# Performance work log

Measured on AMD Instinct MI355X. Metric: run time of the kernel, lower is better.

## Reference

```python
import jax, jax.numpy as jnp
import numpy as np

B, NPG, EPG = 128, 1000, 16000   # graphs, nodes per graph, edges per graph
D, K, C = 128, 64, 10            # assign_dim, clusters, classes


def gcn_conv(x, src, dst, W, b, N):
    """PyG GCNConv: add self-loops, symmetric D^-1/2 (A+I) D^-1/2 normalization."""
    loop = jnp.arange(N, dtype=src.dtype)
    s = jnp.concatenate([src, loop])
    d = jnp.concatenate([dst, loop])
    deg = jax.ops.segment_sum(jnp.ones_like(s, dtype=x.dtype), d, num_segments=N)
    dinv = jnp.where(deg > 0, jax.lax.rsqrt(deg), 0.0)
    xw = x @ W                                   # [N, out]
    msg = xw[s] * (dinv[s] * dinv[d])[:, None]   # gather + scale
    return jax.ops.segment_sum(msg, d, num_segments=N) + b


def setup_inputs() -> dict:
    N, E = B * NPG, B * EPG
    rng = np.random.default_rng(0)
    offs = np.repeat(np.arange(B, dtype=np.int32) * NPG, EPG)
    src = rng.integers(0, NPG, size=E).astype(np.int32) + offs
    dst = rng.integers(0, NPG, size=E).astype(np.int32) + offs
    edge_index = jnp.asarray(np.stack([src, dst]))          # [2, E], within-graph edges
    batch = jnp.repeat(jnp.arange(B, dtype=jnp.int32), NPG)  # [N], sorted graph ids

    ks = jax.random.split(jax.random.key(0), 8)
    sc = 0.05
    x = jax.random.normal(ks[0], (N, D), jnp.float32)
    return {
        "x": x,
        "edge_index": edge_index,
        "batch": batch,
        "W_pre": jax.random.normal(ks[1], (D, D), jnp.float32) * sc,
        "b_pre": jnp.zeros((D,), jnp.float32),
        "W_emb": jax.random.normal(ks[2], (D, D), jnp.float32) * sc,
        "b_emb": jnp.zeros((D,), jnp.float32),
        "W_asn": jax.random.normal(ks[3], (D, K), jnp.float32) * sc,
        "b_asn": jnp.zeros((K,), jnp.float32),
        "W1": jax.random.normal(ks[4], (D, D), jnp.float32) * sc,
        "b1": jnp.zeros((D,), jnp.float32),
        "W2": jax.random.normal(ks[5], (D, C), jnp.float32) * sc,
        "b2": jnp.zeros((C,), jnp.float32),
    }


def reference(x, edge_index, batch, W_pre, b_pre, W_emb, b_emb, W_asn, b_asn, W1, b1, W2, b2):
    N = x.shape[0]
    src, dst = edge_index[0], edge_index[1]

    # pre_conv + ReLU
    h = jax.nn.relu(gcn_conv(x, src, dst, W_pre, b_pre, N))

    # DiffPool: embed and assign GCNs
    NE = jax.nn.relu(gcn_conv(h, src, dst, W_emb, b_emb, N))        # [N, D]
    S = jax.nn.softmax(gcn_conv(h, src, dst, W_asn, b_asn, N), -1)  # [N, K]

    # to_dense_batch (equal-size, batch-sorted graphs -> reshape; mask is all-true)
    NEb = NE.reshape(B, NPG, D)
    Sb = S.reshape(B, NPG, K)

    # to_dense_adj: scatter edges into [B, NPG, NPG]
    g = batch[src]
    si = src - g * NPG
    sj = dst - g * NPG
    A = jnp.zeros((B, NPG, NPG), x.dtype).at[g, si, sj].add(1.0)

    Xp = jnp.einsum("bnk,bnd->bkd", Sb, NEb)          # [B, K, D]
    Ap = jnp.einsum("bnk,bnm,bml->bkl", Sb, A, Sb)    # [B, K, K]

    out = Xp.mean(axis=1)                              # [B, D]
    out = jax.nn.relu(out @ W1 + b1)
    return out @ W2 + b2                               # [B, C]
```

## Files before the change

kernel.cpp:

```cpp
#include <hip/hip_runtime.h>
#include <hip/hip_bf16.h>

#define BG   128
#define NPG  1000
#define EPG  16000
#define DIM  128
#define KCL  64
#define CCL  10
#define NN   (BG*NPG)
#define EE   (BG*EPG)

typedef __attribute__((ext_vector_type(8))) short bf16x8;
typedef __attribute__((ext_vector_type(4))) float f32x4;

__device__ __forceinline__ ushort f2bf(float x) {
    unsigned u = __float_as_uint(x);
    return (ushort)((u + 0x7fffu + ((u >> 16) & 1u)) >> 16);
}
__device__ __forceinline__ float bf2f(ushort h) { return __uint_as_float(((unsigned)h) << 16); }


__global__ __launch_bounds__(256) void count_k(const int* __restrict__ dst, int* __restrict__ cnt) {
    int e = blockIdx.x * 256 + threadIdx.x;
    if (e < EE) atomicAdd(&cnt[dst[e]], 1);
}

__global__ __launch_bounds__(256) void dinv_k(const int* __restrict__ cnt, float* __restrict__ dinv) {
    int n = blockIdx.x * 256 + threadIdx.x;
    if (n < NN) dinv[n] = rsqrtf((float)(cnt[n] + 1));
}

__global__ __launch_bounds__(256) void scan_k(const int* __restrict__ cnt, int* __restrict__ offs) {
    int b = blockIdx.x;
    const int nbase = b * NPG;
    const int ebase = b * EPG;
    __shared__ int sdata[256];
    int running = 0;
    for (int j = 0; j < 4; ++j) {
        int i = j * 256 + threadIdx.x;
        int v = (i < NPG) ? cnt[nbase + i] : 0;
        int x = v;
        sdata[threadIdx.x] = x;
        __syncthreads();
        for (int off = 1; off < 256; off <<= 1) {
            int y = (threadIdx.x >= off) ? sdata[threadIdx.x - off] : 0;
            __syncthreads();
            x += y;
            sdata[threadIdx.x] = x;
            __syncthreads();
        }
        int excl = x - v;
        if (i < NPG) offs[nbase + i] = ebase + running + excl;
        int total = sdata[255];
        __syncthreads();
        running += total;
    }
}

__global__ __launch_bounds__(256) void fill_k(const int* __restrict__ src, const int* __restrict__ dst,
                                              const int* __restrict__ offs, int* __restrict__ fill,
                                              int* __restrict__ bucket) {
    int e = blockIdx.x * 256 + threadIdx.x;
    if (e < EE) {
        int d = dst[e];
        int p = atomicAdd(&fill[d], 1);
        bucket[offs[d] + p] = src[e];
    }
}

__global__ __launch_bounds__(256) void wconv_k(const float* __restrict__ Wa, const float* __restrict__ Wb,
                                               ushort* __restrict__ Wah, ushort* __restrict__ Wal,
                                               ushort* __restrict__ Wbh, ushort* __restrict__ Wbl) {
    int i = blockIdx.x * 256 + threadIdx.x;
    if (i < DIM * DIM) {
        int col = i >> 7, k = i & 127;
        float a = Wa[k * DIM + col];
        ushort ha = f2bf(a);
        Wah[i] = ha; Wal[i] = f2bf(a - bf2f(ha));
        float b = Wb[k * DIM + col];
        ushort hb = f2bf(b);
        Wbh[i] = hb; Wbl[i] = f2bf(b - bf2f(hb));
    }
}

template <bool POOL>
__global__ __launch_bounds__(256) void conv_k(const float* __restrict__ X,
                                              const ushort* __restrict__ Wh, const ushort* __restrict__ Wl,
                                              const float* __restrict__ dinv, const int* __restrict__ offs,
                                              const int* __restrict__ cnt, const int* __restrict__ bucket,
                                              const float* __restrict__ bias,
                                              float* __restrict__ out, float* __restrict__ pooled) {
    __shared__ ushort Ah[64 * DIM];
    __shared__ ushort Al[64 * DIM];

    int p = blockIdx.x;
    int blk = (p & 7) * 250 + (p >> 3);
    int wave = threadIdx.x >> 6, lane = threadIdx.x & 63;
    const int nodeBase = blk * 64;
    const float2* base = (const float2*)X;

    for (int i = 0; i < 16; ++i) {
        int row = wave * 16 + i;
        int n = __builtin_amdgcn_readfirstlane(nodeBase + row);
        float di = dinv[n];
        int o = __builtin_amdgcn_readfirstlane(offs[n]);
        int m = __builtin_amdgcn_readfirstlane(cnt[n]);

        float ax = 0.f, ay = 0.f;
        int jj = 0;
        for (; jj + 4 <= m; jj += 4) {
            int s0 = bucket[o + jj], s1 = bucket[o + jj + 1];
            int s2 = bucket[o + jj + 2], s3 = bucket[o + jj + 3];
            float w0 = dinv[s0], w1 = dinv[s1], w2 = dinv[s2], w3 = dinv[s3];
            float2 v0 = base[(size_t)s0 * 64 + lane];
            float2 v1 = base[(size_t)s1 * 64 + lane];
            float2 v2 = base[(size_t)s2 * 64 + lane];
            float2 v3 = base[(size_t)s3 * 64 + lane];
            ax += w0 * v0.x + w1 * v1.x + w2 * v2.x + w3 * v3.x;
            ay += w0 * v0.y + w1 * v1.y + w2 * v2.y + w3 * v3.y;
        }
        for (; jj < m; ++jj) {
            int s = bucket[o + jj];
            float w = dinv[s];
            float2 v = base[(size_t)s * 64 + lane];
            ax += w * v.x; ay += w * v.y;
        }
        float2 vs = base[(size_t)n * 64 + lane];
        float gx = di * (ax + di * vs.x);
        float gy = di * (ay + di * vs.y);

        int byte = (row * 256 + lane * 4) ^ ((row & 7) << 4);
        ushort hx = f2bf(gx), hy = f2bf(gy);
        *(ushort2*)((char*)Ah + byte) = make_ushort2(hx, hy);
        *(ushort2*)((char*)Al + byte) = make_ushort2(f2bf(gx - bf2f(hx)), f2bf(gy - bf2f(hy)));
    }
    __syncthreads();

    int cr = lane & 15, kg = lane >> 4;
    f32x4 acc[2][4];
#pragma unroll
    for (int ct = 0; ct < 2; ++ct)
#pragma unroll
        for (int st = 0; st < 4; ++st) acc[ct][st] = (f32x4)0.f;

#pragma unroll
    for (int t = 0; t < 4; ++t) {
        int kw = t * 32 + kg * 8;
        bf16x8 bh0 = *(const bf16x8*)&Wh[(wave * 32 + cr) * DIM + kw];
        bf16x8 bl0 = *(const bf16x8*)&Wl[(wave * 32 + cr) * DIM + kw];
        bf16x8 bh1 = *(const bf16x8*)&Wh[(wave * 32 + 16 + cr) * DIM + kw];
        bf16x8 bl1 = *(const bf16x8*)&Wl[(wave * 32 + 16 + cr) * DIM + kw];
#pragma unroll
        for (int st = 0; st < 4; ++st) {
            int row = st * 16 + cr;
            int ab = (row * 256 + t * 64 + kg * 16) ^ ((row & 7) << 4);
            bf16x8 ah = *(const bf16x8*)((const char*)Ah + ab);
            bf16x8 al = *(const bf16x8*)((const char*)Al + ab);
            acc[0][st] = __builtin_amdgcn_mfma_f32_16x16x32_bf16(ah, bh0, acc[0][st], 0, 0, 0);
            acc[0][st] = __builtin_amdgcn_mfma_f32_16x16x32_bf16(ah, bl0, acc[0][st], 0, 0, 0);
            acc[0][st] = __builtin_amdgcn_mfma_f32_16x16x32_bf16(al, bh0, acc[0][st], 0, 0, 0);
            acc[1][st] = __builtin_amdgcn_mfma_f32_16x16x32_bf16(ah, bh1, acc[1][st], 0, 0, 0);
            acc[1][st] = __builtin_amdgcn_mfma_f32_16x16x32_bf16(ah, bl1, acc[1][st], 0, 0, 0);
            acc[1][st] = __builtin_amdgcn_mfma_f32_16x16x32_bf16(al, bh1, acc[1][st], 0, 0, 0);
        }
    }

    if (!POOL) {
#pragma unroll
        for (int ct = 0; ct < 2; ++ct) {
            int col = wave * 32 + ct * 16 + cr;
            float bb = bias[col];
#pragma unroll
            for (int st = 0; st < 4; ++st)
#pragma unroll
                for (int rr = 0; rr < 4; ++rr) {
                    int n = nodeBase + st * 16 + kg * 4 + rr;
                    out[(size_t)n * DIM + col] = fmaxf(acc[ct][st][rr] + bb, 0.f);
                }
        }
    } else {
        int g0 = nodeBase / NPG;
        int bnd = (g0 + 1) * NPG;
#pragma unroll
        for (int ct = 0; ct < 2; ++ct) {
            int col = wave * 32 + ct * 16 + cr;
            float bb = bias[col];
            float s1 = 0.f, s2 = 0.f;
#pragma unroll
            for (int st = 0; st < 4; ++st)
#pragma unroll
                for (int rr = 0; rr < 4; ++rr) {
                    int n = nodeBase + st * 16 + kg * 4 + rr;
                    float v = fmaxf(acc[ct][st][rr] + bb, 0.f);
                    if (n < bnd) s1 += v; else s2 += v;
                }
            s1 += __shfl_xor(s1, 16); s1 += __shfl_xor(s1, 32);
            s2 += __shfl_xor(s2, 16); s2 += __shfl_xor(s2, 32);
            if (kg == 0) {
                atomicAdd(&pooled[g0 * DIM + col], s1);
                if (s2 != 0.f) atomicAdd(&pooled[(g0 + 1) * DIM + col], s2);
            }
        }
    }
}

__global__ __launch_bounds__(128) void mlp_k(const float* __restrict__ pooled,
                                             const float* __restrict__ W1, const float* __restrict__ b1,
                                             const float* __restrict__ W2, const float* __restrict__ b2,
                                             float* __restrict__ out) {
    int g = blockIdx.x;
    int t = threadIdx.x;
    __shared__ float prow[DIM];
    __shared__ float o1[DIM];
    prow[t] = pooled[g * DIM + t] * (1.0f / (float)KCL);
    __syncthreads();
    float acc = b1[t];
#pragma unroll 8
    for (int d = 0; d < DIM; ++d) acc += prow[d] * W1[d * DIM + t];
    o1[t] = fmaxf(acc, 0.f);
    __syncthreads();
    if (t < CCL) {
        float a = b2[t];
#pragma unroll 8
        for (int cc = 0; cc < DIM; ++cc) a += o1[cc] * W2[cc * CCL + t];
        out[g * CCL + t] = a;
    }
}

extern "C" void kernel_launch(void* const* d_in, const int* in_sizes, int n_in,
                              void* d_out, int out_size, void* d_ws, size_t ws_size,
                              hipStream_t stream) {
    const float* x     = (const float*)d_in[0];
    const int*   ei    = (const int*)d_in[1];
    const float* W_pre = (const float*)d_in[3];
    const float* b_pre = (const float*)d_in[4];
    const float* W_emb = (const float*)d_in[5];
    const float* b_emb = (const float*)d_in[6];
    const float* W1    = (const float*)d_in[9];
    const float* b1    = (const float*)d_in[10];
    const float* W2    = (const float*)d_in[11];
    const float* b2    = (const float*)d_in[12];
    float* out = (float*)d_out;

    const int* srcp = ei;
    const int* dstp = ei + EE;

    char* ws = (char*)d_ws;
    size_t off = 0;
    int*    cnt    = (int*)(ws + off);    off += (size_t)NN * 4;
    int*    fill   = (int*)(ws + off);    off += (size_t)NN * 4;
    float*  dinv   = (float*)(ws + off);  off += (size_t)NN * 4;
    int*    offs   = (int*)(ws + off);    off += (size_t)NN * 4;
    float*  pooled = (float*)(ws + off);  off += (size_t)BG * DIM * 4;
    ushort* Wph    = (ushort*)(ws + off); off += (size_t)DIM * DIM * 2;
    ushort* Wpl    = (ushort*)(ws + off); off += (size_t)DIM * DIM * 2;
    ushort* Weh    = (ushort*)(ws + off); off += (size_t)DIM * DIM * 2;
    ushort* Wel    = (ushort*)(ws + off); off += (size_t)DIM * DIM * 2;
    int*    bucket = (int*)(ws + off);    off += (size_t)EE * 4;
    float*  h      = (float*)(ws + off);  off += (size_t)NN * DIM * 4;
    if (ws_size < off) return;

    hipMemsetAsync(cnt, 0, (size_t)NN * 4, stream);
    hipMemsetAsync(fill, 0, (size_t)NN * 4, stream);
    hipMemsetAsync(pooled, 0, (size_t)BG * DIM * 4, stream);

    count_k<<<(EE + 255) / 256, 256, 0, stream>>>(dstp, cnt);
    dinv_k<<<(NN + 255) / 256, 256, 0, stream>>>(cnt, dinv);
    scan_k<<<BG, 256, 0, stream>>>(cnt, offs);
    fill_k<<<(EE + 255) / 256, 256, 0, stream>>>(srcp, dstp, offs, fill, bucket);
    wconv_k<<<(DIM * DIM + 255) / 256, 256, 0, stream>>>(W_pre, W_emb, Wph, Wpl, Weh, Wel);

    conv_k<false><<<NN / 64, 256, 0, stream>>>(x, Wph, Wpl, dinv, offs, cnt, bucket, b_pre, h, nullptr);
    conv_k<true><<<NN / 64, 256, 0, stream>>>(h, Weh, Wel, dinv, offs, cnt, bucket, b_emb, nullptr, pooled);

    mlp_k<<<BG, 128, 0, stream>>>(pooled, W1, b1, W2, b2, out);
}
```

Baseline: 516.6 us.

## Prescale h by dinv, fuse dinv into scan, widen gather to float4

Folds the dinv computation into the scan kernel, which also writes absolute fill positions so fill_k needs neither a separate counter memset nor an offs lookup. The first conv stores h already multiplied by dinv[n], so the second conv's gather skips the per-neighbour dinv loads and multiplies. The gather now has half-waves handle one node each with float4 loads instead of full waves with float2, and the launch bounds request higher occupancy. This trades extra register pressure and a subtler stored-h convention for fewer scattered loads and fewer launches.

```diff
diff --git a/kernel.cpp b/kernel.cpp
--- a/kernel.cpp
+++ b/kernel.cpp
@@ -25,12 +25,8 @@
     if (e < EE) atomicAdd(&cnt[dst[e]], 1);
 }
 
-__global__ __launch_bounds__(256) void dinv_k(const int* __restrict__ cnt, float* __restrict__ dinv) {
-    int n = blockIdx.x * 256 + threadIdx.x;
-    if (n < NN) dinv[n] = rsqrtf((float)(cnt[n] + 1));
-}
-
-__global__ __launch_bounds__(256) void scan_k(const int* __restrict__ cnt, int* __restrict__ offs) {
+__global__ __launch_bounds__(256) void scan_k(const int* __restrict__ cnt, int* __restrict__ offs,
+                                              int* __restrict__ fillpos, float* __restrict__ dinv) {
     int b = blockIdx.x;
     const int nbase = b * NPG;
     const int ebase = b * EPG;
@@ -39,6 +35,7 @@
     for (int j = 0; j < 4; ++j) {
         int i = j * 256 + threadIdx.x;
         int v = (i < NPG) ? cnt[nbase + i] : 0;
+        if (i < NPG) dinv[nbase + i] = rsqrtf((float)(v + 1));
         int x = v;
         sdata[threadIdx.x] = x;
         __syncthreads();
@@ -50,7 +47,11 @@
             __syncthreads();
         }
         int excl = x - v;
-        if (i < NPG) offs[nbase + i] = ebase + running + excl;
+        if (i < NPG) {
+            int o = ebase + running + excl;
+            offs[nbase + i] = o;
+            fillpos[nbase + i] = o;
+        }
         int total = sdata[255];
         __syncthreads();
         running += total;
@@ -58,13 +59,11 @@
 }
 
 __global__ __launch_bounds__(256) void fill_k(const int* __restrict__ src, const int* __restrict__ dst,
-                                              const int* __restrict__ offs, int* __restrict__ fill,
-                                              int* __restrict__ bucket) {
+                                              int* __restrict__ fillpos, int* __restrict__ bucket) {
     int e = blockIdx.x * 256 + threadIdx.x;
     if (e < EE) {
-        int d = dst[e];
-        int p = atomicAdd(&fill[d], 1);
-        bucket[offs[d] + p] = src[e];
+        int p = atomicAdd(&fillpos[dst[e]], 1);
+        bucket[p] = src[e];
     }
 }
 
@@ -83,8 +82,8 @@
     }
 }
 
-template <bool POOL>
-__global__ __launch_bounds__(256) void conv_k(const float* __restrict__ X,
+template <bool SCALE_SRC, bool POOL>
+__global__ __launch_bounds__(256, 5) void conv_k(const float* __restrict__ X,
                                               const ushort* __restrict__ Wh, const ushort* __restrict__ Wl,
                                               const float* __restrict__ dinv, const int* __restrict__ offs,
                                               const int* __restrict__ cnt, const int* __restrict__ bucket,
@@ -95,47 +94,72 @@
 
     int p = blockIdx.x;
     int blk = (p & 7) * 250 + (p >> 3);
-    int wave = threadIdx.x >> 6, lane = threadIdx.x & 63;
+    int tid = threadIdx.x;
     const int nodeBase = blk * 64;
-    const float2* base = (const float2*)X;
-
-    for (int i = 0; i < 16; ++i) {
-        int row = wave * 16 + i;
-        int n = __builtin_amdgcn_readfirstlane(nodeBase + row);
+    const float4* Xv = (const float4*)X;
+
+    int half = tid >> 5, q = tid & 31;
+    for (int i = 0; i < 8; ++i) {
+        int row = i * 8 + half;
+        int n = nodeBase + row;
         float di = dinv[n];
-        int o = __builtin_amdgcn_readfirstlane(offs[n]);
-        int m = __builtin_amdgcn_readfirstlane(cnt[n]);
-
-        float ax = 0.f, ay = 0.f;
+        int o = offs[n];
+        int m = cnt[n];
+
+        float ax = 0.f, ay = 0.f, az = 0.f, aw = 0.f;
         int jj = 0;
         for (; jj + 4 <= m; jj += 4) {
             int s0 = bucket[o + jj], s1 = bucket[o + jj + 1];
             int s2 = bucket[o + jj + 2], s3 = bucket[o + jj + 3];
-            float w0 = dinv[s0], w1 = dinv[s1], w2 = dinv[s2], w3 = dinv[s3];
-            float2 v0 = base[(size_t)s0 * 64 + lane];
-            float2 v1 = base[(size_t)s1 * 64 + lane];
-            float2 v2 = base[(size_t)s2 * 64 + lane];
-            float2 v3 = base[(size_t)s3 * 64 + lane];
-            ax += w0 * v0.x + w1 * v1.x + w2 * v2.x + w3 * v3.x;
-            ay += w0 * v0.y + w1 * v1.y + w2 * v2.y + w3 * v3.y;
+            float4 v0 = Xv[(size_t)s0 * 32 + q];
+            float4 v1 = Xv[(size_t)s1 * 32 + q];
+            float4 v2 = Xv[(size_t)s2 * 32 + q];
+            float4 v3 = Xv[(size_t)s3 * 32 + q];
+            if (SCALE_SRC) {
+                float w0 = dinv[s0], w1 = dinv[s1], w2 = dinv[s2], w3 = dinv[s3];
+                ax += w0 * v0.x + w1 * v1.x + w2 * v2.x + w3 * v3.x;
+                ay += w0 * v0.y + w1 * v1.y + w2 * v2.y + w3 * v3.y;
+                az += w0 * v0.z + w1 * v1.z + w2 * v2.z + w3 * v3.z;
+                aw += w0 * v0.w + w1 * v1.w + w2 * v2.w + w3 * v3.w;
+            } else {
+                ax += (v0.x + v1.x) + (v2.x + v3.x);
+                ay += (v0.y + v1.y) + (v2.y + v3.y);
+                az += (v0.z + v1.z) + (v2.z + v3.z);
+                aw += (v0.w + v1.w) + (v2.w + v3.w);
+            }
         }
         for (; jj < m; ++jj) {
             int s = bucket[o + jj];
-            float w = dinv[s];
-            float2 v = base[(size_t)s * 64 + lane];
-            ax += w * v.x; ay += w * v.y;
-        }
-        float2 vs = base[(size_t)n * 64 + lane];
-        float gx = di * (ax + di * vs.x);
-        float gy = di * (ay + di * vs.y);
-
-        int byte = (row * 256 + lane * 4) ^ ((row & 7) << 4);
-        ushort hx = f2bf(gx), hy = f2bf(gy);
-        *(ushort2*)((char*)Ah + byte) = make_ushort2(hx, hy);
-        *(ushort2*)((char*)Al + byte) = make_ushort2(f2bf(gx - bf2f(hx)), f2bf(gy - bf2f(hy)));
+            float4 v = Xv[(size_t)s * 32 + q];
+            if (SCALE_SRC) {
+                float w = dinv[s];
+                ax += w * v.x; ay += w * v.y; az += w * v.z; aw += w * v.w;
+            } else {
+                ax += v.x; ay += v.y; az += v.z; aw += v.w;
+            }
+        }
+        float4 vs = Xv[(size_t)n * 32 + q];
+        float gx, gy, gz, gw;
+        if (SCALE_SRC) {
+            gx = di * (ax + di * vs.x); gy = di * (ay + di * vs.y);
+            gz = di * (az + di * vs.z); gw = di * (aw + di * vs.w);
+        } else {
+            gx = di * (ax + vs.x); gy = di * (ay + vs.y);
+            gz = di * (az + vs.z); gw = di * (aw + vs.w);
+        }
+
+        int byte = (row * 256 + q * 8) ^ ((row & 7) << 4);
+        ushort4 hi, lo;
+        hi.x = f2bf(gx); lo.x = f2bf(gx - bf2f(hi.x));
+        hi.y = f2bf(gy); lo.y = f2bf(gy - bf2f(hi.y));
+        hi.z = f2bf(gz); lo.z = f2bf(gz - bf2f(hi.z));
+        hi.w = f2bf(gw); lo.w = f2bf(gw - bf2f(hi.w));
+        *(ushort4*)((char*)Ah + byte) = hi;
+        *(ushort4*)((char*)Al + byte) = lo;
     }
     __syncthreads();
 
+    int wave = tid >> 6, lane = tid & 63;
     int cr = lane & 15, kg = lane >> 4;
     f32x4 acc[2][4];
 #pragma unroll
@@ -175,7 +199,7 @@
 #pragma unroll
                 for (int rr = 0; rr < 4; ++rr) {
                     int n = nodeBase + st * 16 + kg * 4 + rr;
-                    out[(size_t)n * DIM + col] = fmaxf(acc[ct][st][rr] + bb, 0.f);
+                    out[(size_t)n * DIM + col] = dinv[n] * fmaxf(acc[ct][st][rr] + bb, 0.f);
                 }
         }
     } else {
@@ -247,31 +271,29 @@
 
     char* ws = (char*)d_ws;
     size_t off = 0;
-    int*    cnt    = (int*)(ws + off);    off += (size_t)NN * 4;
-    int*    fill   = (int*)(ws + off);    off += (size_t)NN * 4;
-    float*  dinv   = (float*)(ws + off);  off += (size_t)NN * 4;
-    int*    offs   = (int*)(ws + off);    off += (size_t)NN * 4;
-    float*  pooled = (float*)(ws + off);  off += (size_t)BG * DIM * 4;
-    ushort* Wph    = (ushort*)(ws + off); off += (size_t)DIM * DIM * 2;
-    ushort* Wpl    = (ushort*)(ws + off); off += (size_t)DIM * DIM * 2;
-    ushort* Weh    = (ushort*)(ws + off); off += (size_t)DIM * DIM * 2;
-    ushort* Wel    = (ushort*)(ws + off); off += (size_t)DIM * DIM * 2;
-    int*    bucket = (int*)(ws + off);    off += (size_t)EE * 4;
-    float*  h      = (float*)(ws + off);  off += (size_t)NN * DIM * 4;
+    int*    cnt     = (int*)(ws + off);    off += (size_t)NN * 4;
+    int*    fillpos = (int*)(ws + off);    off += (size_t)NN * 4;
+    float*  dinv    = (float*)(ws + off);  off += (size_t)NN * 4;
+    int*    offs    = (int*)(ws + off);    off += (size_t)NN * 4;
+    float*  pooled  = (float*)(ws + off);  off += (size_t)BG * DIM * 4;
+    ushort* Wph     = (ushort*)(ws + off); off += (size_t)DIM * DIM * 2;
+    ushort* Wpl     = (ushort*)(ws + off); off += (size_t)DIM * DIM * 2;
+    ushort* Weh     = (ushort*)(ws + off); off += (size_t)DIM * DIM * 2;
+    ushort* Wel     = (ushort*)(ws + off); off += (size_t)DIM * DIM * 2;
+    int*    bucket  = (int*)(ws + off);    off += (size_t)EE * 4;
+    float*  h       = (float*)(ws + off);  off += (size_t)NN * DIM * 4;
     if (ws_size < off) return;
 
     hipMemsetAsync(cnt, 0, (size_t)NN * 4, stream);
-    hipMemsetAsync(fill, 0, (size_t)NN * 4, stream);
     hipMemsetAsync(pooled, 0, (size_t)BG * DIM * 4, stream);
 
     count_k<<<(EE + 255) / 256, 256, 0, stream>>>(dstp, cnt);
-    dinv_k<<<(NN + 255) / 256, 256, 0, stream>>>(cnt, dinv);
-    scan_k<<<BG, 256, 0, stream>>>(cnt, offs);
-    fill_k<<<(EE + 255) / 256, 256, 0, stream>>>(srcp, dstp, offs, fill, bucket);
+    scan_k<<<BG, 256, 0, stream>>>(cnt, offs, fillpos, dinv);
+    fill_k<<<(EE + 255) / 256, 256, 0, stream>>>(srcp, dstp, fillpos, bucket);
     wconv_k<<<(DIM * DIM + 255) / 256, 256, 0, stream>>>(W_pre, W_emb, Wph, Wpl, Weh, Wel);
 
-    conv_k<false><<<NN / 64, 256, 0, stream>>>(x, Wph, Wpl, dinv, offs, cnt, bucket, b_pre, h, nullptr);
-    conv_k<true><<<NN / 64, 256, 0, stream>>>(h, Weh, Wel, dinv, offs, cnt, bucket, b_emb, nullptr, pooled);
+    conv_k<true, false><<<NN / 64, 256, 0, stream>>>(x, Wph, Wpl, dinv, offs, cnt, bucket, b_pre, h, nullptr);
+    conv_k<false, true><<<NN / 64, 256, 0, stream>>>(h, Weh, Wel, dinv, offs, cnt, bucket, b_emb, nullptr, pooled);
 
     mlp_k<<<BG, 128, 0, stream>>>(pooled, W1, b1, W2, b2, out);
 }
```

New measurement: 469.1 us. 1.1x faster.
